# Kernel tuning notes

Measured on AMD Instinct MI355X. Metric: run time of the kernel, lower is better.

## Reference

```python
import jax, jax.numpy as jnp
import numpy as np

N_HEADS = 16
ALIBI_BIAS_MAX = 8


def _alibi_bias(n_heads, seq_len):
    # MPT build_alibi_bias: bias[h, j] = -(seq_len-1-j) * slope_h, arranged [1,H,1,S]
    pos = jnp.arange(1 - seq_len, 1, dtype=jnp.float32).reshape(1, 1, 1, seq_len)
    m = jnp.arange(1, n_heads + 1, dtype=jnp.float32) * (ALIBI_BIAS_MAX / n_heads)
    slopes = (1.0 / jnp.exp2(m)).reshape(1, n_heads, 1, 1)
    return pos * slopes  # [1,H,1,S]


def setup_inputs() -> dict:
    key = jax.random.key(0)
    k1, k2, k3 = jax.random.split(key, 3)
    B, S, D = 1, 2048, 2048
    x = jax.random.normal(k1, (B, S, D), dtype=jnp.float32)
    # Wqkv: Linear(D, 3D, bias=False); out_proj: Linear(D, D, bias=False)
    w_qkv = jax.random.normal(k2, (3 * D, D), dtype=jnp.float32) * (1.0 / np.sqrt(D))
    w_out = jax.random.normal(k3, (D, D), dtype=jnp.float32) * (1.0 / np.sqrt(D))
    return {"x": x, "w_qkv": w_qkv, "w_out": w_out}


def reference(x, w_qkv, w_out):
    B, S, D = x.shape
    H = N_HEADS
    d = D // H
    qkv = x @ w_qkv.T                              # [B,S,3D]
    q, k, v = jnp.split(qkv, 3, axis=-1)
    q = q.reshape(B, S, H, d).transpose(0, 2, 1, 3)  # [B,H,S,d]
    k = k.reshape(B, S, H, d).transpose(0, 2, 1, 3)
    v = v.reshape(B, S, H, d).transpose(0, 2, 1, 3)
    scale = 1.0 / np.sqrt(d)
    scores = jnp.einsum('bhqd,bhkd->bhqk', q, k) * scale  # [B,H,S,S]
    scores = scores + _alibi_bias(H, S)
    min_val = jnp.finfo(scores.dtype).min
    causal = jnp.tril(jnp.ones((S, S), dtype=bool))
    scores = jnp.where(causal[None, None, :, :], scores, min_val)
    probs = jax.nn.softmax(scores.astype(jnp.float32), axis=-1).astype(q.dtype)
    out = jnp.einsum('bhqk,bhkd->bhqd', probs, v)  # [B,H,S,d]
    out = out.transpose(0, 2, 1, 3).reshape(B, S, D)
    return out @ w_out.T
```

## Files before the change

### kernel.cpp

```cpp
#include <hip/hip_runtime.h>

typedef __bf16 bf16;
typedef __bf16 bf16x8 __attribute__((ext_vector_type(8)));
typedef __bf16 bf16x4 __attribute__((ext_vector_type(4)));
typedef float f32x4 __attribute__((ext_vector_type(4)));

#if __has_builtin(__builtin_amdgcn_exp2f)
#define EXP2(x) __builtin_amdgcn_exp2f(x)
#else
#define EXP2(x) exp2f(x)
#endif

__device__ __forceinline__ void gload_lds16(const void* g, void* l) {
  __builtin_amdgcn_global_load_lds(
      (const __attribute__((address_space(1))) void*)g,
      (__attribute__((address_space(3))) void*)l, 16, 0, 0);
}

__global__ __launch_bounds__(256) void cast_f32_bf16(const float* __restrict__ in,
                                                     bf16* __restrict__ out, int n) {
  int i = (blockIdx.x * 256 + threadIdx.x) * 4;
  if (i < n) {
    float4 v = *(const float4*)(in + i);
    bf16x4 o = {(bf16)v.x, (bf16)v.y, (bf16)v.z, (bf16)v.w};
    *(bf16x4*)(out + i) = o;
  }
}

template <int EPI>
__global__ __launch_bounds__(256) void gemm_bt(const bf16* __restrict__ A,
                                               const bf16* __restrict__ B,
                                               float* __restrict__ Cf,
                                               bf16* __restrict__ qb,
                                               bf16* __restrict__ kb,
                                               bf16* __restrict__ vt,
                                               int M, int N, int K) {
  __shared__ bf16 As[128 * 32];
  __shared__ bf16 Bs[128 * 32];
  const int t = threadIdx.x;
  const int w = t >> 6, l = t & 63;
  const int lr = l & 15, lg = l >> 4;
  const int nwg = gridDim.x * gridDim.y;
  int lin = blockIdx.y * gridDim.x + blockIdx.x;
  lin = (lin & 7) * (nwg >> 3) + (lin >> 3);
  const int bn = lin % gridDim.x;
  const int bm = lin / gridDim.x;
  const int wr = w >> 1, wc = w & 1;

  f32x4 acc[4][4] = {};
  const int row0 = t >> 2;
  const int cc0 = (t & 3) * 8;

  for (int k0 = 0; k0 < K; k0 += 32) {
#pragma unroll
    for (int r = 0; r < 2; ++r) {
      const int row = r * 64 + row0;
      gload_lds16(A + (size_t)(bm * 128 + row) * K + k0 + cc0,
                  (char*)As + (r * 256 + w * 64) * 16);
      gload_lds16(B + (size_t)(bn * 128 + row) * K + k0 + cc0,
                  (char*)Bs + (r * 256 + w * 64) * 16);
    }
    __syncthreads();
    bf16x8 af[4], bfr[4];
#pragma unroll
    for (int i = 0; i < 4; ++i) {
      af[i] = *(const bf16x8*)((const char*)As + (wr * 64 + i * 16 + lr) * 64 + lg * 16);
      bfr[i] = *(const bf16x8*)((const char*)Bs + (wc * 64 + i * 16 + lr) * 64 + lg * 16);
    }
#pragma unroll
    for (int mi = 0; mi < 4; ++mi)
#pragma unroll
      for (int ni = 0; ni < 4; ++ni)
        acc[mi][ni] = __builtin_amdgcn_mfma_f32_16x16x32_bf16(af[mi], bfr[ni],
                                                              acc[mi][ni], 0, 0, 0);
    __syncthreads();
  }

  const int mb = bm * 128 + wr * 64 + lg * 4;
  const int nb = bn * 128 + wc * 64 + lr;
  if (EPI == 0) {
#pragma unroll
    for (int mi = 0; mi < 4; ++mi) {
      const int mg = mb + mi * 16;
#pragma unroll
      for (int ni = 0; ni < 4; ++ni) {
        const int ng = nb + ni * 16;
#pragma unroll
        for (int rr = 0; rr < 4; ++rr)
          Cf[(size_t)(mg + rr) * N + ng] = acc[mi][ni][rr];
      }
    }
  } else {
    if (bn * 128 < 4096) {
      bf16* dst = (bn * 128 < 2048) ? qb : kb;
#pragma unroll
      for (int mi = 0; mi < 4; ++mi) {
        const int mg = mb + mi * 16;
#pragma unroll
        for (int ni = 0; ni < 4; ++ni) {
          const int ng = (nb + ni * 16) & 2047;
#pragma unroll
          for (int rr = 0; rr < 4; ++rr)
            dst[(size_t)(mg + rr) * 2048 + ng] = (bf16)acc[mi][ni][rr];
        }
      }
    } else {
#pragma unroll
      for (int mi = 0; mi < 4; ++mi) {
        const int mg = mb + mi * 16;
#pragma unroll
        for (int ni = 0; ni < 4; ++ni) {
          const int dc = nb + ni * 16 - 4096;
          bf16x4 pk = {(bf16)acc[mi][ni][0], (bf16)acc[mi][ni][1],
                       (bf16)acc[mi][ni][2], (bf16)acc[mi][ni][3]};
          *(bf16x4*)(vt + (size_t)dc * 2048 + mg) = pk;
        }
      }
    }
  }
}

__global__ __launch_bounds__(256) void attn_kernel(const bf16* __restrict__ qb,
                                                   const bf16* __restrict__ kb,
                                                   const bf16* __restrict__ vt,
                                                   bf16* __restrict__ out) {
  constexpr int S = 2048, D = 2048;
  __shared__ bf16 Ks[2][64 * 128];
  __shared__ bf16 Vs[2][128 * 64];
  __shared__ bf16 Ps[4][16 * 64];
  const int t = threadIdx.x;
  const int w = t >> 6, l = t & 63;
  const int lr = l & 15, lg = l >> 4;
  const int b = blockIdx.x;
  const int h = b & 15;
  const int qt = (b < 256) ? (31 - (b >> 4)) : ((b - 256) >> 4);
  const int q0 = qt * 64;
  const float slope2 = exp2f(-0.5f * (float)(h + 1)) * 1.4426950408889634f;
  const float scale2 = 0.08838834764831845f * 1.4426950408889634f;

  bf16x8 qf[4];
  {
    const bf16* qrow = qb + (size_t)(q0 + w * 16 + lr) * D + h * 128 + lg * 8;
#pragma unroll
    for (int kk = 0; kk < 4; ++kk) qf[kk] = *(const bf16x8*)(qrow + kk * 32);
  }

  f32x4 ob[8] = {};
  float mrow[4] = {-1e30f, -1e30f, -1e30f, -1e30f};
  float lrow[4] = {0.f, 0.f, 0.f, 0.f};

  const int nt = qt + 1;

  auto stage = [&](int kv0, int bb) {
#pragma unroll
    for (int r = 0; r < 4; ++r) {
      {
        const int krow = r * 16 + (t >> 4);
        const int kcc = t & 15;
        gload_lds16(kb + (size_t)(kv0 + krow) * D + h * 128 + ((kcc ^ (krow & 7)) * 8),
                    (char*)Ks[bb] + (r * 256 + w * 64) * 16);
      }
      {
        const int vrow = r * 32 + (t >> 3);
        const int vcc = t & 7;
        gload_lds16(vt + (size_t)(h * 128 + vrow) * S + kv0 + ((vcc ^ (vrow & 7)) * 8),
                    (char*)Vs[bb] + (r * 256 + w * 64) * 16);
      }
    }
  };

  stage(0, 0);
  int cur = 0;
  for (int tile = 0; tile < nt; ++tile) {
    __syncthreads();
    if (tile + 1 < nt) stage((tile + 1) << 6, cur ^ 1);
    const int kv0 = tile << 6;

    f32x4 sc[4] = {};
#pragma unroll
    for (int jb = 0; jb < 4; ++jb) {
      const int row = jb * 16 + lr;
#pragma unroll
      for (int kk = 0; kk < 4; ++kk) {
        const int byte = row * 256 + ((kk * 64 + lg * 16) ^ ((row & 7) << 4));
        bf16x8 kf = *(const bf16x8*)((const char*)Ks[cur] + byte);
        sc[jb] = __builtin_amdgcn_mfma_f32_16x16x32_bf16(qf[kk], kf, sc[jb], 0, 0, 0);
      }
    }

    float bias[4];
#pragma unroll
    for (int jb = 0; jb < 4; ++jb)
      bias[jb] = slope2 * (float)(kv0 + jb * 16 + lr - (S - 1));
    const bool diag = (tile == nt - 1);
    float xv[4][4], m2r[4];
#pragma unroll
    for (int rr = 0; rr < 4; ++rr) {
#pragma unroll
      for (int jb = 0; jb < 4; ++jb) {
        float v = fmaf(sc[jb][rr], scale2, bias[jb]);
        if (diag && (jb * 16 + lr > w * 16 + lg * 4 + rr)) v = -1e30f;
        xv[rr][jb] = v;
      }
      float m2 = fmaxf(fmaxf(xv[rr][0], xv[rr][1]), fmaxf(xv[rr][2], xv[rr][3]));
      m2 = fmaxf(m2, __shfl_xor(m2, 1));
      m2 = fmaxf(m2, __shfl_xor(m2, 2));
      m2 = fmaxf(m2, __shfl_xor(m2, 4));
      m2 = fmaxf(m2, __shfl_xor(m2, 8));
      m2r[rr] = m2;
    }
    float need = fmaxf(fmaxf(m2r[0] - mrow[0], m2r[1] - mrow[1]),
                       fmaxf(m2r[2] - mrow[2], m2r[3] - mrow[3]));
    if (!__all(need <= 8.0f)) {
#pragma unroll
      for (int rr = 0; rr < 4; ++rr) {
        const float mnew = fmaxf(mrow[rr], m2r[rr]);
        const float cf = EXP2(mrow[rr] - mnew);
        lrow[rr] *= cf;
        mrow[rr] = mnew;
#pragma unroll
        for (int db = 0; db < 8; ++db) ob[db][rr] *= cf;
      }
    }
    char* pbase = (char*)Ps[w];
#pragma unroll
    for (int rr = 0; rr < 4; ++rr) {
      const int prow = lg * 4 + rr;
      const int sw = (prow & 7) << 4;
      float ps = 0.f;
#pragma unroll
      for (int jb = 0; jb < 4; ++jb) {
        const float p = EXP2(xv[rr][jb] - mrow[rr]);
        *(bf16*)(pbase + ((prow * 128 + jb * 32 + lr * 2) ^ sw)) = (bf16)p;
        ps += p;
      }
      lrow[rr] += ps;
    }

    bf16x8 pf[2];
#pragma unroll
    for (int s = 0; s < 2; ++s)
      pf[s] = *(const bf16x8*)(pbase + ((lr * 128 + s * 64 + lg * 16) ^ ((lr & 7) << 4)));
#pragma unroll
    for (int db = 0; db < 8; ++db) {
      const int vrow = db * 16 + lr;
#pragma unroll
      for (int s = 0; s < 2; ++s) {
        const int byte = vrow * 128 + ((s * 64 + lg * 16) ^ ((vrow & 7) << 4));
        bf16x8 vf = *(const bf16x8*)((const char*)Vs[cur] + byte);
        ob[db] = __builtin_amdgcn_mfma_f32_16x16x32_bf16(pf[s], vf, ob[db], 0, 0, 0);
      }
    }
    cur ^= 1;
  }

#pragma unroll
  for (int rr = 0; rr < 4; ++rr) {
    float ls = lrow[rr];
    ls += __shfl_xor(ls, 1);
    ls += __shfl_xor(ls, 2);
    ls += __shfl_xor(ls, 4);
    ls += __shfl_xor(ls, 8);
    const float inv = 1.0f / ls;
    const int mg = q0 + w * 16 + lg * 4 + rr;
#pragma unroll
    for (int db = 0; db < 8; ++db)
      out[(size_t)mg * D + h * 128 + db * 16 + lr] = (bf16)(ob[db][rr] * inv);
  }
}

extern "C" void kernel_launch(void* const* d_in, const int* in_sizes, int n_in,
                              void* d_out, int out_size, void* d_ws, size_t ws_size,
                              hipStream_t stream) {
  (void)in_sizes; (void)n_in; (void)out_size; (void)ws_size;
  const float* x = (const float*)d_in[0];
  const float* wqkv = (const float*)d_in[1];
  const float* wout = (const float*)d_in[2];
  float* out = (float*)d_out;

  bf16* x_bf = (bf16*)d_ws;
  bf16* wqkv_bf = x_bf + (size_t)2048 * 2048;
  bf16* wout_bf = wqkv_bf + (size_t)6144 * 2048;
  bf16* qb = wout_bf + (size_t)2048 * 2048;
  bf16* kb = qb + (size_t)2048 * 2048;
  bf16* vt = kb + (size_t)2048 * 2048;
  bf16* attn = wqkv_bf;

  cast_f32_bf16<<<4096, 256, 0, stream>>>(x, x_bf, 2048 * 2048);
  cast_f32_bf16<<<12288, 256, 0, stream>>>(wqkv, wqkv_bf, 6144 * 2048);
  cast_f32_bf16<<<4096, 256, 0, stream>>>(wout, wout_bf, 2048 * 2048);

  gemm_bt<1><<<dim3(48, 16), 256, 0, stream>>>(x_bf, wqkv_bf, nullptr, qb, kb, vt,
                                               2048, 6144, 2048);
  attn_kernel<<<512, 256, 0, stream>>>(qb, kb, vt, attn);
  gemm_bt<0><<<dim3(16, 16), 256, 0, stream>>>(attn, wout_bf, out, nullptr, nullptr,
                                               nullptr, 2048, 2048, 2048);
}
```

Baseline: 208.2 us.

## Deepen GEMM K tile to 64 with k-major LDS layout and split-K output projection

```diff
diff --git a/kernel.cpp b/kernel.cpp
--- a/kernel.cpp
+++ b/kernel.cpp
@@ -27,16 +27,28 @@
   }
 }
 
+__global__ __launch_bounds__(256) void add_f32(float* __restrict__ out,
+                                               const float* __restrict__ p, int n) {
+  int i = (blockIdx.x * 256 + threadIdx.x) * 4;
+  if (i < n) {
+    f32x4 a = *(const f32x4*)(out + i);
+    f32x4 b = *(const f32x4*)(p + i);
+    a += b;
+    *(f32x4*)(out + i) = a;
+  }
+}
+
 template <int EPI>
 __global__ __launch_bounds__(256) void gemm_bt(const bf16* __restrict__ A,
                                                const bf16* __restrict__ B,
                                                float* __restrict__ Cf,
+                                               float* __restrict__ Cf2,
                                                bf16* __restrict__ qb,
                                                bf16* __restrict__ kb,
                                                bf16* __restrict__ vt,
-                                               int M, int N, int K) {
-  __shared__ bf16 As[128 * 32];
-  __shared__ bf16 Bs[128 * 32];
+                                               int M, int N, int K, int klen) {
+  __shared__ bf16 As[8 * 1024];
+  __shared__ bf16 Bs[8 * 1024];
   const int t = threadIdx.x;
   const int w = t >> 6, l = t & 63;
   const int lr = l & 15, lg = l >> 4;
@@ -46,39 +58,45 @@
   const int bn = lin % gridDim.x;
   const int bm = lin / gridDim.x;
   const int wr = w >> 1, wc = w & 1;
+  const int kbase = blockIdx.z * klen;
 
   f32x4 acc[4][4] = {};
-  const int row0 = t >> 2;
-  const int cc0 = (t & 3) * 8;
-
-  for (int k0 = 0; k0 < K; k0 += 32) {
-#pragma unroll
-    for (int r = 0; r < 2; ++r) {
-      const int row = r * 64 + row0;
-      gload_lds16(A + (size_t)(bm * 128 + row) * K + k0 + cc0,
+
+  for (int k0 = kbase; k0 < kbase + klen; k0 += 64) {
+#pragma unroll
+    for (int r = 0; r < 4; ++r) {
+      const int c = r * 256 + t;
+      const int kc = c >> 7, row = c & 127;
+      gload_lds16(A + (size_t)(bm * 128 + row) * K + k0 + kc * 8,
                   (char*)As + (r * 256 + w * 64) * 16);
-      gload_lds16(B + (size_t)(bn * 128 + row) * K + k0 + cc0,
+      gload_lds16(B + (size_t)(bn * 128 + row) * K + k0 + kc * 8,
                   (char*)Bs + (r * 256 + w * 64) * 16);
     }
     __syncthreads();
-    bf16x8 af[4], bfr[4];
-#pragma unroll
-    for (int i = 0; i < 4; ++i) {
-      af[i] = *(const bf16x8*)((const char*)As + (wr * 64 + i * 16 + lr) * 64 + lg * 16);
-      bfr[i] = *(const bf16x8*)((const char*)Bs + (wc * 64 + i * 16 + lr) * 64 + lg * 16);
-    }
-#pragma unroll
-    for (int mi = 0; mi < 4; ++mi)
-#pragma unroll
-      for (int ni = 0; ni < 4; ++ni)
-        acc[mi][ni] = __builtin_amdgcn_mfma_f32_16x16x32_bf16(af[mi], bfr[ni],
-                                                              acc[mi][ni], 0, 0, 0);
+#pragma unroll
+    for (int kk = 0; kk < 2; ++kk) {
+      bf16x8 af[4], bfr[4];
+#pragma unroll
+      for (int i = 0; i < 4; ++i) {
+        af[i] = *(const bf16x8*)((const char*)As + (kk * 4 + lg) * 2048 +
+                                 (wr * 64 + i * 16 + lr) * 16);
+        bfr[i] = *(const bf16x8*)((const char*)Bs + (kk * 4 + lg) * 2048 +
+                                  (wc * 64 + i * 16 + lr) * 16);
+      }
+#pragma unroll
+      for (int mi = 0; mi < 4; ++mi)
+#pragma unroll
+        for (int ni = 0; ni < 4; ++ni)
+          acc[mi][ni] = __builtin_amdgcn_mfma_f32_16x16x32_bf16(af[mi], bfr[ni],
+                                                                acc[mi][ni], 0, 0, 0);
+    }
     __syncthreads();
   }
 
   const int mb = bm * 128 + wr * 64 + lg * 4;
   const int nb = bn * 128 + wc * 64 + lr;
   if (EPI == 0) {
+    float* dst = blockIdx.z ? Cf2 : Cf;
 #pragma unroll
     for (int mi = 0; mi < 4; ++mi) {
       const int mg = mb + mi * 16;
@@ -87,7 +105,7 @@
         const int ng = nb + ni * 16;
 #pragma unroll
         for (int rr = 0; rr < 4; ++rr)
-          Cf[(size_t)(mg + rr) * N + ng] = acc[mi][ni][rr];
+          dst[(size_t)(mg + rr) * N + ng] = acc[mi][ni][rr];
       }
     }
   } else {
@@ -285,14 +303,17 @@
   bf16* kb = qb + (size_t)2048 * 2048;
   bf16* vt = kb + (size_t)2048 * 2048;
   bf16* attn = wqkv_bf;
+  float* part1 = (float*)qb;
 
   cast_f32_bf16<<<4096, 256, 0, stream>>>(x, x_bf, 2048 * 2048);
   cast_f32_bf16<<<12288, 256, 0, stream>>>(wqkv, wqkv_bf, 6144 * 2048);
   cast_f32_bf16<<<4096, 256, 0, stream>>>(wout, wout_bf, 2048 * 2048);
 
-  gemm_bt<1><<<dim3(48, 16), 256, 0, stream>>>(x_bf, wqkv_bf, nullptr, qb, kb, vt,
-                                               2048, 6144, 2048);
+  gemm_bt<1><<<dim3(48, 16, 1), 256, 0, stream>>>(x_bf, wqkv_bf, nullptr, nullptr,
+                                                  qb, kb, vt, 2048, 6144, 2048, 2048);
   attn_kernel<<<512, 256, 0, stream>>>(qb, kb, vt, attn);
-  gemm_bt<0><<<dim3(16, 16), 256, 0, stream>>>(attn, wout_bf, out, nullptr, nullptr,
-                                               nullptr, 2048, 2048, 2048);
-}
+  gemm_bt<0><<<dim3(16, 16, 2), 256, 0, stream>>>(attn, wout_bf, out, part1,
+                                                  nullptr, nullptr, nullptr,
+                                                  2048, 2048, 2048, 1024);
+  add_f32<<<4096, 256, 0, stream>>>(out, part1, 2048 * 2048);
+}
```

Measured after the change: 265.5 us. 1.28x slower.
